# Kernel tuning notes

Hardware: AMD Instinct MI355X
Metric: run time of the kernel (lower is better)

## Reference

```python
import jax, jax.numpy as jnp
import numpy as np

B, S, D, DFF = 8, 2048, 1024, 4096

def setup_inputs() -> dict:
    key = jax.random.key(0)
    ks = jax.random.split(key, 11)
    s = 0.02
    return {
        "x":  jax.random.normal(ks[0], (B, S, D), dtype=jnp.float32),
        "Wq": jax.random.normal(ks[1], (D, D), dtype=jnp.float32) * s,
        "bq": jnp.zeros((D,), dtype=jnp.float32),
        "Wk": jax.random.normal(ks[2], (D, D), dtype=jnp.float32) * s,
        "bk": jnp.zeros((D,), dtype=jnp.float32),
        "Wv": jax.random.normal(ks[3], (D, D), dtype=jnp.float32) * s,
        "bv": jnp.zeros((D,), dtype=jnp.float32),
        "W1": jax.random.normal(ks[4], (DFF, D), dtype=jnp.float32) * s,
        "b1": jnp.zeros((DFF,), dtype=jnp.float32),
        "W2": jax.random.normal(ks[5], (D, DFF), dtype=jnp.float32) * s,
        "b2": jnp.zeros((D,), dtype=jnp.float32),
    }

def reference(x, Wq, bq, Wk, bk, Wv, bv, W1, b1, W2, b2):
    # qkv projections (torch Linear: x @ W.T + b)
    q = jnp.einsum('bsd,ed->bse', x, Wq) + bq
    k = jnp.einsum('bsd,ed->bse', x, Wk) + bk
    v = jnp.einsum('bsd,ed->bse', x, Wv) + bv
    # single-head scaled dot-product attention with causal mask (decoder=True)
    scale = 1.0 / jnp.sqrt(jnp.asarray(q.shape[-1], q.dtype))
    scores = jnp.einsum('bqd,bkd->bqk', q, k) * scale  # (B,S,S)
    causal = jnp.tril(jnp.ones((scores.shape[-2], scores.shape[-1]), dtype=bool))
    scores = jnp.where(causal, scores, jnp.asarray(-jnp.inf, scores.dtype))
    attn = jax.nn.softmax(scores, axis=-1)
    attn_out = jnp.einsum('bqk,bkd->bqd', attn, v)
    # MLP: linear_2(gelu(linear_1(.)))  — exact (erf) GELU as in torch default
    h = jax.nn.gelu(jnp.einsum('bsd,fd->bsf', attn_out, W1) + b1, approximate=False)
    return jnp.einsum('bsf,df->bsd', h, W2) + b2
```

## Files before the change

kernel.cpp:

```cpp
#include <hip/hip_runtime.h>
#include <hip/hip_bf16.h>

#define NB   8
#define SS   2048
#define DD   1024
#define DFFN 4096
#define MTOT (NB*SS)

typedef unsigned short u16;
typedef __attribute__((ext_vector_type(4))) float f32x4;
typedef __attribute__((ext_vector_type(8))) short bf16x8;
typedef __attribute__((ext_vector_type(4))) int i32x4;
typedef __attribute__((ext_vector_type(4))) unsigned short u16x4;
typedef __attribute__((ext_vector_type(8))) unsigned short u16x8;

__device__ __forceinline__ u16 f2bf(float f) {
  union { float f; unsigned u; } c; c.f = f;
  unsigned r = c.u + 0x7FFFu + ((c.u >> 16) & 1u);
  return (u16)(r >> 16);
}

__device__ __forceinline__ void gload16(const void* g, void* l) {
  __builtin_amdgcn_global_load_lds(
      (const __attribute__((address_space(1))) void*)(unsigned long long)g,
      (__attribute__((address_space(3))) void*)(unsigned)(unsigned long long)l,
      16, 0, 0);
}

__device__ __forceinline__ bf16x8 dsr128(unsigned addr) {
  i32x4 r;
  asm volatile("ds_read_b128 %0, %1" : "=v"(r) : "v"(addr));
  return __builtin_bit_cast(bf16x8, r);
}

template<int EBIAS, int EGELU, int ESCALE, int EROWSCALE, int OUTMODE, int CSKIP, int CK>
__global__ __launch_bounds__(256, 4)
void gemm128(const u16* __restrict__ A, const u16* __restrict__ B,
             const float* __restrict__ bias0, const float* __restrict__ bias1,
             const float* __restrict__ bias2, const float* __restrict__ rowscale,
             void* __restrict__ C0, void* __restrict__ C1, void* __restrict__ C2,
             int K, int lda, int ldb, int ldc, float scale,
             long long sA, long long sB, long long sC, int sRS)
{
  __shared__ __align__(1024) u16 smem[24576];

  const int gx = gridDim.x, gy = gridDim.y;
  const int nwg = gx * gy;
  const int orig = blockIdx.y * gx + blockIdx.x;
  const int q = nwg >> 3, r = nwg & 7;
  const int xcd = orig & 7, pos0 = orig >> 3;
  const int wg = (xcd < r ? xcd * (q + 1) : r * (q + 1) + (xcd - r) * q) + pos0;
  int bx, by;
  if ((gx & 3) == 0) {
    const int rr = wg % (gy << 2);
    bx = (wg / (gy << 2)) * 4 + (rr & 3);
    by = rr >> 2;
  } else {
    bx = wg % gx; by = wg / gx;
  }
  const int row0 = by * 128, col0 = bx * 128;
  if (CSKIP && col0 > row0 + 127) return;

  const int z = blockIdx.z;
  A += (size_t)z * sA;
  B += (size_t)z * sB;

  int nkt = K >> 5;
  if (CK) { int lim = (row0 + 128) >> 5; if (lim < nkt) nkt = lim; }

  const int tid  = threadIdx.x;
  const int wid  = tid >> 6;
  const int lane = tid & 63;
  const int wr = wid >> 1, wc = wid & 1;

  const int srow = wid * 16 + (lane >> 2);
  const int sunit = (lane & 3) ^ ((lane >> 3) & 3);
  const char* gA = (const char*)A + ((size_t)(row0 + srow) * lda + sunit * 8) * 2;
  const char* gB = (const char*)B + ((size_t)(col0 + srow) * ldb + sunit * 8) * 2;
  const size_t ldab = (size_t)64 * lda * 2;
  const size_t ldbb = (size_t)64 * ldb * 2;

  #define STG(t2, bo) { char* lb = (char*)smem + (bo); size_t kb = (size_t)(t2) * 64; \
      gload16(gA + kb,        lb + wid * 1024);                                       \
      gload16(gA + kb + ldab, lb + 4096 + wid * 1024);                                \
      gload16(gB + kb,        lb + 8192 + wid * 1024);                                \
      gload16(gB + kb + ldbb, lb + 8192 + 4096 + wid * 1024); }

  const int fr = lane & 15;
  const int ks16 = ((lane >> 4) & 3) * 16;
  const int xm = ((lane >> 1) & 3) << 4;
  const unsigned sbase = (unsigned)(unsigned long long)(void*)smem;

  f32x4 acc[4][4] = {};

  STG(0, 0); STG(1, 16384);
  asm volatile("s_waitcnt vmcnt(4)");
  asm volatile("s_barrier" ::: "memory");

  unsigned cbo = 0, sbo = 32768;

  #define KSTEP_BODY(WAITN)                                                    \
    bf16x8 af[4], bf[4];                                                       \
    _Pragma("unroll") for (int m = 0; m < 4; ++m)                              \
      af[m] = dsr128(sbase + cbo + (((wr * 64 + m * 16 + fr) * 64 + ks16) ^ xm)); \
    _Pragma("unroll") for (int n = 0; n < 4; ++n)                              \
      bf[n] = dsr128(sbase + cbo + ((8192 + (wc * 64 + n * 16 + fr) * 64 + ks16) ^ xm)); \
    asm volatile("s_waitcnt lgkmcnt(0)");                                      \
    __builtin_amdgcn_sched_barrier(0);                                         \
    __builtin_amdgcn_s_setprio(1);                                             \
    _Pragma("unroll") for (int m = 0; m < 4; ++m)                              \
      _Pragma("unroll") for (int n = 0; n < 4; ++n)                            \
        acc[m][n] = __builtin_amdgcn_mfma_f32_16x16x32_bf16(af[m], bf[n], acc[m][n], 0, 0, 0); \
    __builtin_amdgcn_s_setprio(0);                                             \
    asm volatile("s_waitcnt vmcnt(" #WAITN ")");                               \
    asm volatile("s_barrier" ::: "memory");                                    \
    cbo += 16384; if (cbo == 49152) cbo = 0;                                   \
    sbo += 16384; if (sbo == 49152) sbo = 0;

  for (int t = 0; t < nkt - 2; ++t) {
    STG(t + 2, sbo);
    KSTEP_BODY(4)
  }
  { KSTEP_BODY(0) }
  { KSTEP_BODY(0) }
  #undef KSTEP_BODY
  #undef STG

  char* sm = (char*)smem;
  const int r4 = (lane >> 4) * 4;
  const int sel  = (OUTMODE == 3) ? (col0 >> 10) : 0;
  const int oc0  = (OUTMODE == 3) ? (col0 & 1023) : col0;
  const float* bias = (OUTMODE == 3) ? (sel == 0 ? bias0 : sel == 1 ? bias1 : bias2)
                                     : bias0;

  if (OUTMODE == 1) {
#pragma unroll
    for (int p = 0; p < 2; ++p) {
      if (wc == p) {
#pragma unroll
        for (int n = 0; n < 4; ++n) {
          const int col = oc0 + wc * 64 + n * 16 + fr;
          const int pb = (n * 16 + fr) * 4;
          float bia = EBIAS ? bias[col] : 0.0f;
#pragma unroll
          for (int m = 0; m < 4; ++m) {
#pragma unroll
            for (int j = 0; j < 4; ++j) {
              const int line = wr * 64 + m * 16 + r4 + j;
              float xv = acc[m][n][j];
              if (EBIAS)     xv += bia;
              if (ESCALE)    xv *= scale;
              if (EROWSCALE) xv *= rowscale[z * sRS + row0 + line];
              if (EGELU)     xv = 0.5f * xv * (1.0f + erff(xv * 0.70710678118f));
              *(float*)(sm + ((line * 256 + pb) ^ ((line & 7) << 4))) = xv;
            }
          }
        }
      }
      __syncthreads();
      float* Cb = (float*)C0 + (size_t)z * sC;
#pragma unroll
      for (int i = 0; i < 8; ++i) {
        const int o = i * 4096 + tid * 16;
        const int line = o >> 8, ps = o & 255;
        f32x4 v = *(const f32x4*)(sm + ((line * 256 + ps) ^ ((line & 7) << 4)));
        *(f32x4*)((char*)(Cb + (size_t)(row0 + line) * ldc + oc0 + p * 64) + ps) = v;
      }
      __syncthreads();
    }
  } else if (OUTMODE == 3 && sel == 2) {
#pragma unroll
    for (int n = 0; n < 4; ++n) {
      const int line = wc * 64 + n * 16 + fr;
      float bia = EBIAS ? bias[oc0 + line] : 0.0f;
#pragma unroll
      for (int m = 0; m < 4; ++m) {
        const int rb = wr * 64 + m * 16 + r4;
        u16x4 pk;
#pragma unroll
        for (int j = 0; j < 4; ++j) pk[j] = f2bf(acc[m][n][j] + bia);
        *(u16x4*)(sm + ((line * 256 + rb * 2) ^ ((line & 7) << 4))) = pk;
      }
    }
    __syncthreads();
    u16* Cb = (u16*)C2 + (size_t)(row0 >> 11) * (DD * SS) + (row0 & (SS - 1));
#pragma unroll
    for (int i = 0; i < 8; ++i) {
      const int o = i * 4096 + tid * 16;
      const int line = o >> 8, ps = o & 255;
      f32x4 v = *(const f32x4*)(sm + ((line * 256 + ps) ^ ((line & 7) << 4)));
      *(f32x4*)((char*)(Cb + (size_t)(oc0 + line) * SS) + ps) = v;
    }
  } else {
#pragma unroll
    for (int n = 0; n < 4; ++n) {
      const int col = oc0 + wc * 64 + n * 16 + fr;
      const int pc = (wc * 64 + n * 16 + fr) * 2;
      float bia = EBIAS ? bias[col] : 0.0f;
#pragma unroll
      for (int m = 0; m < 4; ++m) {
#pragma unroll
        for (int j = 0; j < 4; ++j) {
          const int line = wr * 64 + m * 16 + r4 + j;
          float xv = acc[m][n][j];
          if (EBIAS)     xv += bia;
          if (ESCALE)    xv *= scale;
          if (EROWSCALE) xv *= rowscale[z * sRS + row0 + line];
          if (EGELU)     xv = 0.5f * xv * (1.0f + erff(xv * 0.70710678118f));
          u16 u;
          if (OUTMODE == 2) { union { u16 s; _Float16 h; } cu; cu.h = (_Float16)xv; u = cu.s; }
          else u = f2bf(xv);
          *(u16*)(sm + ((line * 256 + pc) ^ ((line & 7) << 4))) = u;
        }
      }
    }
    __syncthreads();
    u16* Cb = (u16*)(OUTMODE == 3 ? (sel ? C1 : C0) : C0) + (size_t)z * sC + oc0;
#pragma unroll
    for (int i = 0; i < 8; ++i) {
      const int o = i * 4096 + tid * 16;
      const int line = o >> 8, ps = o & 255;
      f32x4 v = *(const f32x4*)(sm + ((line * 256 + ps) ^ ((line & 7) << 4)));
      *(f32x4*)((char*)(Cb + (size_t)(row0 + line) * ldc) + ps) = v;
    }
  }
}

__global__ __launch_bounds__(256) void cvt_all_k(
    const float* __restrict__ x,  const float* __restrict__ wq,
    const float* __restrict__ wk, const float* __restrict__ wv,
    const float* __restrict__ w1, const float* __restrict__ w2,
    u16* __restrict__ out_x, u16* __restrict__ out_w)
{
  const int i = blockIdx.x * 256 + threadIdx.x;
  const float* src; int off; u16* dst; int dofs;
  if (i < 4194304)      { src = x;  off = i;           dst = out_x; dofs = i; }
  else if (i < 4456448) { src = wq; off = i - 4194304; dst = out_w; dofs = i - 4194304; }
  else if (i < 4718592) { src = wk; off = i - 4456448; dst = out_w; dofs = i - 4194304; }
  else if (i < 4980736) { src = wv; off = i - 4718592; dst = out_w; dofs = i - 4194304; }
  else if (i < 6029312) { src = w1; off = i - 4980736; dst = out_w; dofs = i - 4194304; }
  else                  { src = w2; off = i - 6029312; dst = out_w; dofs = i - 4194304; }
  float4 v = ((const float4*)src)[off];
  u16x4 o;
  o.x = f2bf(v.x); o.y = f2bf(v.y); o.z = f2bf(v.z); o.w = f2bf(v.w);
  ((u16x4*)dst)[dofs] = o;
}

__global__ __launch_bounds__(256) void softmax_k(u16* __restrict__ sc, float* __restrict__ rinv, int rows0) {
  const int widx = blockIdx.x * 4 + (threadIdx.x >> 6);
  const int lane = threadIdx.x & 63;
  u16* row = sc + (size_t)widx * SS;
  const int L = (widx & (SS - 1)) + 1;
  float mx = -1e30f;
  for (int k = 0; k < 4; ++k) {
    const int j0 = k * 512 + lane * 8;
    if (j0 < L) {
      u16x8 v = *(const u16x8*)(row + j0);
      int lim = L - j0; if (lim > 8) lim = 8;
#pragma unroll
      for (int e = 0; e < 8; ++e) {
        if (e < lim) { union { u16 u; _Float16 h; } c; c.u = v[e]; mx = fmaxf(mx, (float)c.h); }
      }
    }
  }
#pragma unroll
  for (int o = 32; o >= 1; o >>= 1) mx = fmaxf(mx, __shfl_xor(mx, o));
  float sacc = 0.0f;
  for (int k = 0; k < 4; ++k) {
    const int j0 = k * 512 + lane * 8;
    u16x8 v = *(const u16x8*)(row + j0);
    u16x8 w;
#pragma unroll
    for (int e = 0; e < 8; ++e) {
      const int j = j0 + e;
      float ev = 0.0f;
      if (j < L) { union { u16 u; _Float16 h; } c; c.u = v[e]; ev = __expf((float)c.h - mx); sacc += ev; }
      w[e] = f2bf(ev);
    }
    *(u16x8*)(row + j0) = w;
  }
#pragma unroll
  for (int o = 32; o >= 1; o >>= 1) sacc += __shfl_xor(sacc, o);
  if (lane == 0) rinv[rows0 + widx] = 1.0f / sacc;
}

extern "C" void kernel_launch(void* const* d_in, const int* in_sizes, int n_in,
                              void* d_out, int out_size, void* d_ws, size_t ws_size,
                              hipStream_t stream) {
  const float* x  = (const float*)d_in[0];
  const float* Wq = (const float*)d_in[1];
  const float* bq = (const float*)d_in[2];
  const float* Wk = (const float*)d_in[3];
  const float* bk = (const float*)d_in[4];
  const float* Wv = (const float*)d_in[5];
  const float* bv = (const float*)d_in[6];
  const float* W1 = (const float*)d_in[7];
  const float* b1 = (const float*)d_in[8];
  const float* W2 = (const float*)d_in[9];
  const float* b2 = (const float*)d_in[10];

  char* ws = (char*)d_ws;
  u16*  Qb   = (u16*)(ws);
  u16*  Kb   = (u16*)(ws + 33554432);
  u16*  Vtb  = (u16*)(ws + 67108864);
  u16*  big  = (u16*)(ws + 100663296);
  float* rinv = (float*)(ws + 167772160);
  u16*  Wcat = (u16*)(ws + 167772160 + 65536);
  u16*  W1b  = Wcat + 3 * DD * DD;
  u16*  W2b  = W1b + DFFN * DD;
  u16*  xb   = big;
  u16*  att  = Qb;
  u16*  h    = Kb;

  cvt_all_k<<<27648, 256, 0, stream>>>(x, Wq, Wk, Wv, W1, W2, xb, Wcat);

  gemm128<1,0,0,0,3,0,0><<<dim3(3 * DD / 128, MTOT / 128), 256, 0, stream>>>(
      xb, Wcat, bq, bk, bv, nullptr, (void*)Qb, (void*)Kb, (void*)Vtb,
      DD, DD, DD, DD, 0.f, 0, 0, 0, 0);

  gemm128<0,0,1,0,2,1,0><<<dim3(SS/128, SS/128, NB), 256, 0, stream>>>(
      Qb, Kb, nullptr, nullptr, nullptr, nullptr, (void*)big, nullptr, nullptr,
      DD, DD, DD, SS, 0.03125f,
      (long long)SS * DD, (long long)SS * DD, (long long)SS * SS, 0);
  softmax_k<<<NB * SS / 4, 256, 0, stream>>>(big, rinv, 0);
  gemm128<0,0,0,1,0,0,1><<<dim3(DD/128, SS/128, NB), 256, 0, stream>>>(
      big, Vtb, nullptr, nullptr, nullptr, rinv,
      (void*)att, nullptr, nullptr,
      SS, SS, SS, DD, 0.f,
      (long long)SS * SS, (long long)DD * SS, (long long)SS * DD, SS);

  gemm128<1,1,0,0,0,0,0><<<dim3(DFFN/128, MTOT/128), 256, 0, stream>>>(
      att, W1b, b1, nullptr, nullptr, nullptr,
      (void*)h, nullptr, nullptr,
      DD, DD, DD, DFFN, 0.f, 0, 0, 0, 0);
  gemm128<1,0,0,0,1,0,0><<<dim3(DD/128, MTOT/128), 256, 0, stream>>>(
      h, W2b, b2, nullptr, nullptr, nullptr,
      (void*)d_out, nullptr, nullptr,
      DFFN, DFFN, DFFN, DD, 0.f, 0, 0, 0, 0);
}
```

Baseline: 679.4 us.

## Add specialized K=64 double-buffered GEMM kernel for the W1+GELU projection

Adds a dedicated 128x128 tile GEMM that stages 64-wide K slices into LDS with double buffering and an XCD-aware, column-grouped workgroup remap. The first MLP projection (with bias and erf GELU) now uses it instead of the generic templated gemm128. The goal is fewer barriers per K step, better L2 reuse across XCDs, and two workgroups per CU. The cost is a larger shared-memory footprint and register pressure from the 2-occupancy launch bound.

Result: slower. 722.2 us (+6.3%).

```diff
diff --git a/kernel.cpp b/kernel.cpp
--- a/kernel.cpp
+++ b/kernel.cpp
@@ -223,6 +223,129 @@
       f32x4 v = *(const f32x4*)(sm + ((line * 256 + ps) ^ ((line & 7) << 4)));
       *(f32x4*)((char*)(Cb + (size_t)(row0 + line) * ldc) + ps) = v;
     }
+  }
+}
+
+template<int EGELU>
+__global__ __launch_bounds__(256, 2)
+void gemm128k64(const u16* __restrict__ A, const u16* __restrict__ B,
+                const float* __restrict__ bias, void* __restrict__ C,
+                int K, int lda, int ldb, int ldc)
+{
+  __shared__ __align__(1024) u16 smem[32768];
+
+  const int gx = gridDim.x, gy = gridDim.y;
+  const int nwg = gx * gy;
+  const int orig = blockIdx.y * gx + blockIdx.x;
+  const int q = nwg >> 3, r = nwg & 7;
+  const int xcd = orig & 7, pos0 = orig >> 3;
+  const int wg = (xcd < r ? xcd * (q + 1) : r * (q + 1) + (xcd - r) * q) + pos0;
+  int bx, by;
+  if ((gx & 3) == 0) {
+    const int rr = wg % (gy << 2);
+    bx = (wg / (gy << 2)) * 4 + (rr & 3);
+    by = rr >> 2;
+  } else {
+    bx = wg % gx; by = wg / gx;
+  }
+  const int row0 = by * 128, col0 = bx * 128;
+
+  const int nkt = K >> 6;
+  const int tid = threadIdx.x, wid = tid >> 6, lane = tid & 63;
+  const int wr = wid >> 1, wc = wid & 1;
+  const int fr = lane & 15, s = lane >> 4;
+
+  const int l8 = lane >> 3;
+  const int u8 = (lane & 7) ^ (l8 & 7);
+  const char* gA = (const char*)A + ((size_t)(row0 + wid * 32 + l8) * lda + u8 * 8) * 2;
+  const char* gB = (const char*)B + ((size_t)(col0 + wid * 32 + l8) * ldb + u8 * 8) * 2;
+  const size_t lda8 = (size_t)8 * lda * 2;
+  const size_t ldb8 = (size_t)8 * ldb * 2;
+  const unsigned sbase = (unsigned)(unsigned long long)(void*)smem;
+
+  #define STG64(t2, bo) { char* la = (char*)smem + (bo) + wid * 4096;          \
+      char* lb2 = (char*)smem + (bo) + 16384 + wid * 4096;                     \
+      size_t kb = (size_t)(t2) * 128;                                          \
+      gload16(gA + kb,            la);                                         \
+      gload16(gA + kb +     lda8, la + 1024);                                  \
+      gload16(gA + kb + 2 * lda8, la + 2048);                                  \
+      gload16(gA + kb + 3 * lda8, la + 3072);                                  \
+      gload16(gB + kb,            lb2);                                        \
+      gload16(gB + kb +     ldb8, lb2 + 1024);                                 \
+      gload16(gB + kb + 2 * ldb8, lb2 + 2048);                                 \
+      gload16(gB + kb + 3 * ldb8, lb2 + 3072); }
+
+  #define RDAF(h) _Pragma("unroll") for (int m = 0; m < 4; ++m)                \
+      af[m] = dsr128(sbase + cbo + (unsigned)((wr * 64 + m * 16 + fr) * 128 +  \
+                     ((((h) * 4 + s) ^ (fr & 7)) << 4)));
+  #define RDBF(h) _Pragma("unroll") for (int n = 0; n < 4; ++n)                \
+      bf[n] = dsr128(sbase + cbo + 16384u + (unsigned)((wc * 64 + n * 16 + fr) * 128 + \
+                     ((((h) * 4 + s) ^ (fr & 7)) << 4)));
+
+  f32x4 acc[4][4] = {};
+
+  STG64(0, 0);
+  asm volatile("s_waitcnt vmcnt(0)");
+  asm volatile("s_barrier" ::: "memory");
+
+  unsigned cbo = 0;
+  for (int t = 0; t < nkt; ++t) {
+    if (t + 1 < nkt) STG64(t + 1, cbo ^ 16384u ^ 49152u);
+    bf16x8 af[4], bf[4];
+    RDAF(0); RDBF(0);
+    asm volatile("s_waitcnt lgkmcnt(0)");
+    __builtin_amdgcn_sched_barrier(0);
+    __builtin_amdgcn_s_setprio(1);
+#pragma unroll
+    for (int m = 0; m < 4; ++m)
+#pragma unroll
+      for (int n = 0; n < 4; ++n)
+        acc[m][n] = __builtin_amdgcn_mfma_f32_16x16x32_bf16(af[m], bf[n], acc[m][n], 0, 0, 0);
+    __builtin_amdgcn_s_setprio(0);
+    RDAF(1); RDBF(1);
+    asm volatile("s_waitcnt lgkmcnt(0)");
+    __builtin_amdgcn_sched_barrier(0);
+    __builtin_amdgcn_s_setprio(1);
+#pragma unroll
+    for (int m = 0; m < 4; ++m)
+#pragma unroll
+      for (int n = 0; n < 4; ++n)
+        acc[m][n] = __builtin_amdgcn_mfma_f32_16x16x32_bf16(af[m], bf[n], acc[m][n], 0, 0, 0);
+    __builtin_amdgcn_s_setprio(0);
+    asm volatile("s_waitcnt vmcnt(0)");
+    asm volatile("s_barrier" ::: "memory");
+    cbo ^= 32768u;
+  }
+  #undef STG64
+  #undef RDAF
+  #undef RDBF
+
+  char* sm = (char*)smem;
+  const int r4 = s * 4;
+#pragma unroll
+  for (int n = 0; n < 4; ++n) {
+    const int col = col0 + wc * 64 + n * 16 + fr;
+    const int pc = (wc * 64 + n * 16 + fr) * 2;
+    const float bia = bias[col];
+#pragma unroll
+    for (int m = 0; m < 4; ++m) {
+#pragma unroll
+      for (int j = 0; j < 4; ++j) {
+        const int line = wr * 64 + m * 16 + r4 + j;
+        float xv = acc[m][n][j] + bia;
+        if (EGELU) xv = 0.5f * xv * (1.0f + erff(xv * 0.70710678118f));
+        *(u16*)(sm + ((line * 256 + pc) ^ ((line & 7) << 4))) = f2bf(xv);
+      }
+    }
+  }
+  __syncthreads();
+  u16* Cb = (u16*)C + col0;
+#pragma unroll
+  for (int i = 0; i < 8; ++i) {
+    const int o = i * 4096 + tid * 16;
+    const int line = o >> 8, ps = o & 255;
+    f32x4 v = *(const f32x4*)(sm + ((line * 256 + ps) ^ ((line & 7) << 4)));
+    *(f32x4*)((char*)(Cb + (size_t)(row0 + line) * ldc) + ps) = v;
   }
 }
 
@@ -329,10 +452,8 @@
       SS, SS, SS, DD, 0.f,
       (long long)SS * SS, (long long)DD * SS, (long long)SS * DD, SS);
 
-  gemm128<1,1,0,0,0,0,0><<<dim3(DFFN/128, MTOT/128), 256, 0, stream>>>(
-      att, W1b, b1, nullptr, nullptr, nullptr,
-      (void*)h, nullptr, nullptr,
-      DD, DD, DD, DFFN, 0.f, 0, 0, 0, 0);
+  gemm128k64<1><<<dim3(DFFN/128, MTOT/128), 256, 0, stream>>>(
+      att, W1b, b1, (void*)h, DD, DD, DD, DFFN);
   gemm128<1,0,0,0,1,0,0><<<dim3(DD/128, MTOT/128), 256, 0, stream>>>(
       h, W2b, b2, nullptr, nullptr, nullptr,
       (void*)d_out, nullptr, nullptr,
```
